# Optimization experiments

Measured on AMD Instinct MI355X. Metric: run time of the kernel, lower is better.

Reference implementation:

```python
import jax, jax.numpy as jnp
import numpy as np

B, LQ, LK = 16, 1024, 2048
E, F, A = 512, 256, 512


def setup_inputs() -> dict:
    key = jax.random.key(0)
    ks = jax.random.split(key, 8)
    s_e = 1.0 / np.sqrt(E)
    s_f = 1.0 / np.sqrt(F)
    s_a = 1.0 / np.sqrt(A)
    return {
        "lstm_embeddings": jax.random.normal(ks[0], (B, LQ, E), jnp.float32),
        "optical_flow_features": jax.random.normal(ks[1], (B, LK, F), jnp.float32),
        "Wq": jax.random.normal(ks[2], (E, A), jnp.float32) * s_e,
        "bq": jnp.zeros((A,), jnp.float32),
        "Wk": jax.random.normal(ks[3], (F, A), jnp.float32) * s_f,
        "bk": jnp.zeros((A,), jnp.float32),
        "Wv": jax.random.normal(ks[4], (F, A), jnp.float32) * s_f,
        "bv": jnp.zeros((A,), jnp.float32),
        "Wo": jax.random.normal(ks[5], (A, E), jnp.float32) * s_a,
        "bo": jnp.zeros((E,), jnp.float32),
    }


def reference(lstm_embeddings, optical_flow_features, Wq, bq, Wk, bk, Wv, bv, Wo, bo):
    # Linear projections (x @ W + b), matching nn.Linear with W stored as [in, out]
    q = lstm_embeddings @ Wq + bq            # [B, LQ, A]
    k = optical_flow_features @ Wk + bk      # [B, LK, A]
    v = optical_flow_features @ Wv + bv      # [B, LK, A]
    # NOTE: original module does NOT scale scores by 1/sqrt(A) — stay faithful.
    scores = jnp.einsum("bqa,bka->bqk", q, k)      # [B, LQ, LK]
    weights = jax.nn.softmax(scores, axis=-1)
    context = jnp.einsum("bqk,bka->bqa", weights, v)  # [B, LQ, A]
    return context @ Wo + bo                          # [B, LQ, E]
```

## Files before the change

kernel.cpp:

```cpp
#include <hip/hip_runtime.h>


#define DEV static __device__ __forceinline__

typedef __attribute__((ext_vector_type(8))) short s8v;
typedef __attribute__((ext_vector_type(8))) _Float16 h8v;
typedef __attribute__((ext_vector_type(4))) _Float16 h4v;
typedef __attribute__((ext_vector_type(4))) float f4v;
typedef __attribute__((ext_vector_type(16))) float f16f;
typedef __attribute__((ext_vector_type(4))) float float4v;
typedef unsigned short u16;
typedef unsigned int u32;

constexpr int BB = 16;
constexpr int LQ = 1024;
constexpr int LK = 2048;
constexpr int E = 512;
constexpr int F = 256;

DEV u16 f2bf(float x) {
    u32 u = __builtin_bit_cast(u32, x);
    u += 0x7fff + ((u >> 16) & 1);
    return (u16)(u >> 16);
}
DEV float bf2f(u16 h) { return __builtin_bit_cast(float, (u32)h << 16); }

DEV f4v MF(s8v a, s8v b, f4v c) {
    return __builtin_amdgcn_mfma_f32_16x16x32_bf16(a, b, c, 0, 0, 0);
}
DEV f4v MF16(h8v a, h8v b, f4v c) {
    return __builtin_amdgcn_mfma_f32_16x16x32_f16(a, b, c, 0, 0, 0);
}
DEV f16f MF32(h8v a, h8v b, f16f c) {
    return __builtin_amdgcn_mfma_f32_32x32x16_f16(a, b, c, 0, 0, 0);
}

__global__ __launch_bounds__(256) void wgemm(
    const float* __restrict__ Wq, const float* __restrict__ bq,
    const float* __restrict__ Wk, const float* __restrict__ Wv,
    const float* __restrict__ bv, const float* __restrict__ Wo,
    const float* __restrict__ bo,
    u16* __restrict__ Mhb, u16* __restrict__ Ntb,
    float* __restrict__ wvec, float* __restrict__ cvec)
{
    const int bi = blockIdx.x;
    const int tid = threadIdx.x;
    if (bi >= 64) {
        if (bi == 64) {
            const float* r = Wk + (size_t)tid * 512;
            float s = 0.f;
#pragma unroll 4
            for (int a = 0; a < 512; a += 4) {
                float4v v = *(const float4v*)(r + a);
                float4v bb = *(const float4v*)(bq + a);
                s += v[0] * bb[0] + v[1] * bb[1] + v[2] * bb[2] + v[3] * bb[3];
            }
            wvec[tid] = s;
        } else {
            int e = (bi - 65) * 256 + tid;
            float s = bo[e];
#pragma unroll 4
            for (int a = 0; a < 512; ++a) s += bv[a] * Wo[(size_t)a * 512 + e];
            cvec[e] = s;
        }
        return;
    }
    const bool ntm = bi >= 32;
    const int bj = ntm ? bi - 32 : bi;
    const int m0 = ntm ? (bj >> 2) * 64 : (bj >> 3) * 64;
    const int n0 = ntm ? (bj & 3) * 64 : (bj & 7) * 64;
    const float* Ag = ntm ? Wo : Wk;
    const float* Bg = ntm ? Wv : Wq;

    __shared__ u16 Ash[64][40], Asl[64][40];
    __shared__ u16 Bsh[64][40], Bsl[64][40];

    const int w = tid >> 6, lane = tid & 63;
    const int g = lane >> 4, qn = lane & 15;
    const int wr = w & 1, wc = w >> 1;

    f4v acc[2][2];
#pragma unroll
    for (int i = 0; i < 2; ++i)
#pragma unroll
        for (int j = 0; j < 2; ++j) acc[i][j] = (f4v){0.f, 0.f, 0.f, 0.f};

    for (int k0 = 0; k0 < 512; k0 += 32) {
        __syncthreads();
        if (!ntm) {
            int r = tid & 63, c = (tid >> 6) * 8;
            const float* s = Ag + (size_t)(m0 + r) * 512 + k0 + c;
            float4v v0 = *(const float4v*)s, v1 = *(const float4v*)(s + 4);
            short hh[8], ll[8];
#pragma unroll
            for (int i = 0; i < 8; ++i) {
                float x = (i < 4) ? v0[i] : v1[i - 4];
                u16 h = f2bf(x);
                hh[i] = (short)h;
                ll[i] = (short)f2bf(x - bf2f(h));
            }
            *(s8v*)&Ash[r][c] = (s8v){hh[0],hh[1],hh[2],hh[3],hh[4],hh[5],hh[6],hh[7]};
            *(s8v*)&Asl[r][c] = (s8v){ll[0],ll[1],ll[2],ll[3],ll[4],ll[5],ll[6],ll[7]};
        } else {
            int k = tid >> 3, mc = (tid & 7) * 8;
            const float* s = Ag + (size_t)(k0 + k) * 512 + m0 + mc;
            float4v v0 = *(const float4v*)s, v1 = *(const float4v*)(s + 4);
#pragma unroll
            for (int i = 0; i < 8; ++i) {
                float x = (i < 4) ? v0[i] : v1[i - 4];
                u16 h = f2bf(x);
                Ash[mc + i][k] = h;
                Asl[mc + i][k] = f2bf(x - bf2f(h));
            }
        }
        {
            int r = tid & 63, c = (tid >> 6) * 8;
            const float* s = Bg + (size_t)(n0 + r) * 512 + k0 + c;
            float4v v0 = *(const float4v*)s, v1 = *(const float4v*)(s + 4);
            short hh[8], ll[8];
#pragma unroll
            for (int i = 0; i < 8; ++i) {
                float x = (i < 4) ? v0[i] : v1[i - 4];
                u16 h = f2bf(x);
                hh[i] = (short)h;
                ll[i] = (short)f2bf(x - bf2f(h));
            }
            *(s8v*)&Bsh[r][c] = (s8v){hh[0],hh[1],hh[2],hh[3],hh[4],hh[5],hh[6],hh[7]};
            *(s8v*)&Bsl[r][c] = (s8v){ll[0],ll[1],ll[2],ll[3],ll[4],ll[5],ll[6],ll[7]};
        }
        __syncthreads();

        s8v ah[2], al[2], bh[2], bl[2];
#pragma unroll
        for (int mt = 0; mt < 2; ++mt) {
            ah[mt] = *(const s8v*)&Ash[wr * 32 + mt * 16 + qn][g * 8];
            al[mt] = *(const s8v*)&Asl[wr * 32 + mt * 16 + qn][g * 8];
        }
#pragma unroll
        for (int nt = 0; nt < 2; ++nt) {
            bh[nt] = *(const s8v*)&Bsh[wc * 32 + nt * 16 + qn][g * 8];
            bl[nt] = *(const s8v*)&Bsl[wc * 32 + nt * 16 + qn][g * 8];
        }
#pragma unroll
        for (int mt = 0; mt < 2; ++mt)
#pragma unroll
            for (int nt = 0; nt < 2; ++nt) {
                acc[mt][nt] = MF(ah[mt], bh[nt], acc[mt][nt]);
                acc[mt][nt] = MF(ah[mt], bl[nt], acc[mt][nt]);
                acc[mt][nt] = MF(al[mt], bh[nt], acc[mt][nt]);
            }
    }

#pragma unroll
    for (int mt = 0; mt < 2; ++mt)
#pragma unroll
        for (int nt = 0; nt < 2; ++nt)
#pragma unroll
            for (int r = 0; r < 4; ++r) {
                int gm = m0 + wr * 32 + mt * 16 + 4 * g + r;
                int gn = n0 + wc * 32 + nt * 16 + qn;
                float v = acc[mt][nt][r];
                if (!ntm) {
                    size_t off = (size_t)((gn >> 5) * 16 + (gm >> 4)) * 512 +
                                 (gm & 15) * 8 + ((gn >> 3) & 3) * 128 + (gn & 7);
                    Mhb[off] = __builtin_bit_cast(u16, (_Float16)v);
                } else {
                    size_t off = (size_t)((gn >> 5) * 32 + (gm >> 4)) * 512 +
                                 (gm & 15) * 8 + ((gn >> 3) & 3) * 128 + (gn & 7);
                    Ntb[off] = __builtin_bit_cast(u16, (_Float16)v);
                }
            }
}

__global__ __launch_bounds__(256) void prep16s(
    const float* __restrict__ y, _Float16* __restrict__ yA,
    _Float16* __restrict__ yB)
{
    __shared__ float Y[32][260];
    const int tid = threadIdx.x;
    const int b = blockIdx.y, t = blockIdx.x;
    const float* src = y + ((size_t)b * LK + t * 32) * F;
#pragma unroll
    for (int i = 0; i < 8; ++i) {
        int base = i * 1024 + tid * 4;
        int k = base >> 8, f = base & 255;
        *(float4v*)&Y[k][f] = *(const float4v*)(src + base);
    }
    __syncthreads();
    size_t tb = (size_t)(b * 64 + t) * 8192;
#pragma unroll
    for (int i = 0; i < 4; ++i) {
        int c = i * 256 + tid;
        int k = c & 31, hi = (c >> 5) & 1, fs = c >> 6;
        int f0 = fs * 16 + hi * 8;
        float4v v0 = *(const float4v*)&Y[k][f0];
        float4v v1 = *(const float4v*)&Y[k][f0 + 4];
        h8v v;
#pragma unroll
        for (int j = 0; j < 4; ++j) { v[j] = (_Float16)v0[j]; v[4 + j] = (_Float16)v1[j]; }
        *(h8v*)(yA + tb + (size_t)c * 8) = v;
    }
#pragma unroll
    for (int i = 0; i < 4; ++i) {
        int c = i * 256 + tid;
        int fl = c & 31, hi = (c >> 5) & 1, frag = c >> 6;
        int ft = frag >> 1, ks = frag & 1;
        int f = ft * 32 + fl, k0 = ks * 16 + hi * 8;
        h8v v;
#pragma unroll
        for (int j = 0; j < 8; ++j) v[j] = (_Float16)Y[k0 + j][f];
        *(h8v*)(yB + tb + (size_t)c * 8) = v;
    }
}

__global__ __launch_bounds__(256) void qprime4(
    const float* __restrict__ x, const u16* __restrict__ Mhb,
    const float* __restrict__ wv, _Float16* __restrict__ q16)
{
    __shared__ _Float16 Xs[2][128][40];
    const int tid = threadIdx.x, w = tid >> 6, lane = tid & 63;
    const int g = lane >> 4, qn = lane & 15;
    const int m0 = blockIdx.x * 128;
    const int nh = blockIdx.y * 8;
    const int srow = tid >> 1, scol = (tid & 1) * 16;
    const _Float16* Mh = (const _Float16*)Mhb;

    f4v acc[2][8];
#pragma unroll
    for (int i = 0; i < 2; ++i)
#pragma unroll
        for (int j = 0; j < 8; ++j) acc[i][j] = (f4v){0.f, 0.f, 0.f, 0.f};

    float4v a0, a1, a2, a3;
    auto LDA = [&](int k0) {
        const float* s = x + (size_t)(m0 + srow) * 512 + k0 + scol;
        a0 = *(const float4v*)s;      a1 = *(const float4v*)(s + 4);
        a2 = *(const float4v*)(s + 8); a3 = *(const float4v*)(s + 12);
    };
    auto STA = [&](int buf) {
        h8v v0, v1;
#pragma unroll
        for (int j = 0; j < 4; ++j) {
            v0[j] = (_Float16)a0[j]; v0[4 + j] = (_Float16)a1[j];
            v1[j] = (_Float16)a2[j]; v1[4 + j] = (_Float16)a3[j];
        }
        *(h8v*)&Xs[buf][srow][scol] = v0;
        *(h8v*)&Xs[buf][srow][scol + 8] = v1;
    };

    LDA(0); STA(0); LDA(32);
    __syncthreads();

    for (int t = 0; t < 16; ++t) {
        const int cur = t & 1;
        h8v af[2];
#pragma unroll
        for (int mt = 0; mt < 2; ++mt)
            af[mt] = *(const h8v*)&Xs[cur][(w * 2 + mt) * 16 + qn][g * 8];
        const int fb = t * 16 + nh;
#pragma unroll
        for (int nt = 0; nt < 8; ++nt) {
            h8v bf = *(const h8v*)(Mh + (size_t)(fb + nt) * 512 + lane * 8);
            acc[0][nt] = MF16(af[0], bf, acc[0][nt]);
            acc[1][nt] = MF16(af[1], bf, acc[1][nt]);
        }
        if (t < 15) {
            STA(cur ^ 1);
            if (t < 14) LDA((t + 2) * 32);
            __syncthreads();
        }
    }

#pragma unroll
    for (int mt = 0; mt < 2; ++mt)
#pragma unroll
        for (int nt = 0; nt < 8; ++nt) {
            int col = (nh + nt) * 16 + qn;
            float wvc = wv[col];
#pragma unroll
            for (int r = 0; r < 4; ++r) {
                int row = m0 + w * 32 + mt * 16 + 4 * g + r;
                q16[(size_t)row * 256 + col] = (_Float16)(acc[mt][nt][r] + wvc);
            }
        }
}

__global__ __launch_bounds__(512) void flash3(
    const _Float16* __restrict__ q16, const _Float16* __restrict__ yA,
    const _Float16* __restrict__ yB, _Float16* __restrict__ part,
    float* __restrict__ ml)
{
    __shared__ _Float16 Asb[8192];
    __shared__ _Float16 Bsb[8192];
    __shared__ _Float16 Pls[8][1024];

    const int tid = threadIdx.x;
    const int w = tid >> 6, lane = tid & 63;
    const int q32 = lane & 31, hi = lane >> 5;

    int id = blockIdx.x;
    int xcd = id & 7, slot = id >> 3;
    int grp = xcd + 8 * (slot >> 2);
    int qb = slot & 3;
    int b = grp >> 2, z = grp & 3;
    const int qw = qb * 256 + w * 32;

    h8v qf[16];
    {
        const _Float16* qp = q16 + ((size_t)b * LQ + qw + q32) * 256 + hi * 8;
#pragma unroll
        for (int s = 0; s < 16; ++s) qf[s] = *(const h8v*)(qp + s * 16);
    }
    f16f ctx[8];
#pragma unroll
    for (int i = 0; i < 8; ++i) ctx[i] = (f16f){};
    float mrun = -3.0e38f, lrun = 0.f;

    const size_t tbe = (size_t)(b * 64 + z * 16) * 8192;
    h8v sA0, sA1, sB0, sB1;
    auto LD = [&](int t) {
        const h8v* pa = (const h8v*)(yA + tbe + (size_t)t * 8192);
        const h8v* pb = (const h8v*)(yB + tbe + (size_t)t * 8192);
        sA0 = pa[tid]; sA1 = pa[tid + 512];
        sB0 = pb[tid]; sB1 = pb[tid + 512];
    };
    auto ST = [&]() {
        ((h8v*)Asb)[tid] = sA0; ((h8v*)Asb)[tid + 512] = sA1;
        ((h8v*)Bsb)[tid] = sB0; ((h8v*)Bsb)[tid + 512] = sB1;
    };

    LD(0); ST(); LD(1);
    __syncthreads();

    for (int t = 0; t < 16; ++t) {
        f16f S = (f16f){};
#pragma unroll
        for (int fs = 0; fs < 16; ++fs) {
            h8v a = *(const h8v*)(Asb + fs * 512 + lane * 8);
            S = MF32(a, qf[fs], S);
        }
        float mt = S[0];
#pragma unroll
        for (int r = 1; r < 16; ++r) mt = fmaxf(mt, S[r]);
        mt = fmaxf(mt, __shfl_xor(mt, 32));
        if (!__all(mt <= mrun + 8.f)) {
            float mnew = fmaxf(mrun, mt);
            float alpha = __expf(mrun - mnew);
            lrun *= alpha;
#pragma unroll
            for (int r = 0; r < 16; ++r) {
                int qr = (r & 3) + 8 * (r >> 2) + 4 * hi;
                float ar = __shfl(alpha, qr);
#pragma unroll
                for (int ft = 0; ft < 8; ++ft) ctx[ft][r] *= ar;
            }
            mrun = mnew;
        }
        float p[16], ps = 0.f;
#pragma unroll
        for (int r = 0; r < 16; ++r) { p[r] = __expf(S[r] - mrun); ps += p[r]; }
        ps += __shfl_xor(ps, 32);
        lrun += ps;
        {
            _Float16* pw = &Pls[w][0];
#pragma unroll
            for (int r2 = 0; r2 < 4; ++r2) {
                h4v pk = (h4v){(_Float16)p[4 * r2], (_Float16)p[4 * r2 + 1],
                               (_Float16)p[4 * r2 + 2], (_Float16)p[4 * r2 + 3]};
                *(h4v*)(pw + (r2 >> 1) * 512 + (r2 & 1) * 256 + q32 * 8 + hi * 4) = pk;
            }
        }
#pragma unroll
        for (int ks = 0; ks < 2; ++ks) {
            h8v pa = *(const h8v*)(&Pls[w][ks * 512] + lane * 8);
#pragma unroll
            for (int ft = 0; ft < 8; ++ft) {
                h8v bf = *(const h8v*)(Bsb + (ft * 2 + ks) * 512 + lane * 8);
                ctx[ft] = MF32(pa, bf, ctx[ft]);
            }
        }
        __syncthreads();
        if (t < 15) {
            ST();
            if (t < 14) LD(t + 2);
            __syncthreads();
        }
    }

    float linv = 1.f / lrun;
    _Float16* pp = part + ((size_t)z * (BB * LQ) + (size_t)b * LQ + qw) * 256;
#pragma unroll
    for (int r = 0; r < 16; ++r) {
        int qr = (r & 3) + 8 * (r >> 2) + 4 * hi;
        float ir = __shfl(linv, qr);
#pragma unroll
        for (int ft = 0; ft < 8; ++ft)
            pp[(size_t)qr * 256 + ft * 32 + q32] = (_Float16)(ctx[ft][r] * ir);
    }
    if (hi == 0) {
        size_t mi = (size_t)z * (BB * LQ) + (size_t)b * LQ + qw + q32;
        ml[2 * mi + 0] = mrun;
        ml[2 * mi + 1] = lrun;
    }
}

__global__ __launch_bounds__(256) void gemm2c(
    const _Float16* __restrict__ part, const float* __restrict__ ml,
    const u16* __restrict__ Ntb, const float* __restrict__ cvec,
    float* __restrict__ out)
{
    __shared__ _Float16 Asb[64][40];
    __shared__ float scl[64][4];
    const int tid = threadIdx.x;
    const int w = tid >> 6, lane = tid & 63;
    const int g = lane >> 4, qn = lane & 15;
    const int wr = w >> 1, wc = w & 1;
    const int m0 = blockIdx.x * 64, e0 = blockIdx.y * 256;
    constexpr size_t PL = (size_t)BB * LQ * F;
    constexpr size_t PR = (size_t)BB * LQ;

    if (tid < 64) {
        size_t i = m0 + tid;
        float m0v = ml[2 * i], l0v = ml[2 * i + 1];
        float m1v = ml[2 * (PR + i)], l1v = ml[2 * (PR + i) + 1];
        float m2v = ml[2 * (2 * PR + i)], l2v = ml[2 * (2 * PR + i) + 1];
        float m3v = ml[2 * (3 * PR + i)], l3v = ml[2 * (3 * PR + i) + 1];
        float M = fmaxf(fmaxf(m0v, m1v), fmaxf(m2v, m3v));
        float e0v = __expf(m0v - M), e1v = __expf(m1v - M);
        float e2v = __expf(m2v - M), e3v = __expf(m3v - M);
        float inv = 1.f / (l0v * e0v + l1v * e1v + l2v * e2v + l3v * e3v);
        scl[tid][0] = l0v * e0v * inv;
        scl[tid][1] = l1v * e1v * inv;
        scl[tid][2] = l2v * e2v * inv;
        scl[tid][3] = l3v * e3v * inv;
    }

    f4v acc[2][8];
#pragma unroll
    for (int i = 0; i < 2; ++i)
#pragma unroll
        for (int j = 0; j < 8; ++j) acc[i][j] = (f4v){0.f, 0.f, 0.f, 0.f};

    for (int k0 = 0; k0 < F; k0 += 32) {
        __syncthreads();
        {
            int r = tid & 63, c = (tid >> 6) * 8;
            size_t base = (size_t)(m0 + r) * F + k0 + c;
            h8v p0 = *(const h8v*)(part + base);
            h8v p1 = *(const h8v*)(part + PL + base);
            h8v p2 = *(const h8v*)(part + 2 * PL + base);
            h8v p3 = *(const h8v*)(part + 3 * PL + base);
            float s0 = scl[r][0], s1 = scl[r][1], s2 = scl[r][2], s3 = scl[r][3];
#pragma unroll
            for (int i = 0; i < 8; ++i) {
                float v = (float)p0[i] * s0 + (float)p1[i] * s1 +
                          (float)p2[i] * s2 + (float)p3[i] * s3;
                Asb[r][c + i] = (_Float16)v;
            }
        }
        __syncthreads();

        h8v ah[2], bh[8];
#pragma unroll
        for (int mt = 0; mt < 2; ++mt)
            ah[mt] = *(const h8v*)&Asb[wr * 32 + mt * 16 + qn][g * 8];
        int eb = (e0 + wc * 128) >> 4;
#pragma unroll
        for (int nt = 0; nt < 8; ++nt)
            bh[nt] = *(const h8v*)((const _Float16*)Ntb +
                     (size_t)((k0 >> 5) * 32 + eb + nt) * 512 + lane * 8);
#pragma unroll
        for (int mt = 0; mt < 2; ++mt)
#pragma unroll
            for (int nt = 0; nt < 8; ++nt)
                acc[mt][nt] = MF16(ah[mt], bh[nt], acc[mt][nt]);
    }

#pragma unroll
    for (int mt = 0; mt < 2; ++mt)
#pragma unroll
        for (int nt = 0; nt < 8; ++nt)
#pragma unroll
            for (int r = 0; r < 4; ++r) {
                int gm = m0 + wr * 32 + mt * 16 + 4 * g + r;
                int gn = e0 + wc * 128 + nt * 16 + qn;
                out[(size_t)gm * E + gn] = acc[mt][nt][r] + cvec[gn];
            }
}

extern "C" void kernel_launch(void* const* d_in, const int* in_sizes, int n_in,
                              void* d_out, int out_size, void* d_ws, size_t ws_size,
                              hipStream_t stream)
{
    const float* x  = (const float*)d_in[0];
    const float* y  = (const float*)d_in[1];
    const float* Wq = (const float*)d_in[2];
    const float* bq = (const float*)d_in[3];
    const float* Wk = (const float*)d_in[4];
    const float* Wv = (const float*)d_in[6];
    const float* bv = (const float*)d_in[7];
    const float* Wo = (const float*)d_in[8];
    const float* bo = (const float*)d_in[9];
    float* out = (float*)d_out;

    char* ws = (char*)d_ws;
    size_t off = 0;
    auto alloc = [&](size_t bytes) -> char* {
        char* p = ws + off;
        off = (off + bytes + 255) & ~(size_t)255;
        return p;
    };
    u16* Mhb  = (u16*)alloc(sizeof(u16) * F * E);
    float* wvec = (float*)alloc(sizeof(float) * F);
    float* cvec = (float*)alloc(sizeof(float) * E);
    u16* Ntb  = (u16*)alloc(sizeof(u16) * E * F);
    _Float16* q16 = (_Float16*)alloc(sizeof(u16) * (size_t)BB * LQ * F);
    _Float16* yA  = (_Float16*)alloc(sizeof(u16) * (size_t)BB * LK * F);
    _Float16* yB  = (_Float16*)alloc(sizeof(u16) * (size_t)BB * LK * F);
    _Float16* part = (_Float16*)alloc(sizeof(u16) * 4 * (size_t)BB * LQ * F);
    float* ml = (float*)alloc(sizeof(float) * 2 * 4 * (size_t)BB * LQ);
    (void)ws_size; (void)in_sizes; (void)n_in; (void)out_size;

    wgemm<<<dim3(67), dim3(256), 0, stream>>>(
        Wq, bq, Wk, Wv, bv, Wo, bo, Mhb, Ntb, wvec, cvec);
    prep16s<<<dim3(LK / 32, BB), dim3(256), 0, stream>>>(y, yA, yB);
    qprime4<<<dim3(BB * LQ / 128, 2), dim3(256), 0, stream>>>(x, Mhb, wvec, q16);
    flash3<<<dim3(256), dim3(512), 0, stream>>>(q16, yA, yB, part, ml);
    gemm2c<<<dim3(BB * LQ / 64, E / 256), dim3(256), 0, stream>>>(
        part, ml, Ntb, cvec, out);
}
```

Before: 138.7 us.

## Merge weight and y-prep kernels; double-buffer flash tiles via global_load_lds

The weight GEMM kernel and the y fp16 conversion kernel are fused into one launch, so a kernel boundary and the small serial weight work are removed. The flash attention kernel now stages two key tiles per step into double-buffered LDS using direct global-to-LDS loads, issued one stage ahead. This replaces the register-staged load/store with one barrier per pair of tiles, aiming to overlap memory with MFMA work. In exchange LDS use grows to about 144KB, which may limit occupancy, and the code relies on the async loads finishing before the single barrier.

```diff
diff --git a/kernel.cpp b/kernel.cpp
--- a/kernel.cpp
+++ b/kernel.cpp
@@ -35,7 +35,15 @@
     return __builtin_amdgcn_mfma_f32_32x32x16_f16(a, b, c, 0, 0, 0);
 }
 
-__global__ __launch_bounds__(256) void wgemm(
+DEV void gll16(const _Float16* g, _Float16* l) {
+    __builtin_amdgcn_global_load_lds(
+        (const __attribute__((address_space(1))) u32*)g,
+        (__attribute__((address_space(3))) u32*)l, 16, 0, 0);
+}
+
+__global__ __launch_bounds__(256) void prew(
+    const float* __restrict__ y, _Float16* __restrict__ yA,
+    _Float16* __restrict__ yB,
     const float* __restrict__ Wq, const float* __restrict__ bq,
     const float* __restrict__ Wk, const float* __restrict__ Wv,
     const float* __restrict__ bv, const float* __restrict__ Wo,
@@ -43,10 +51,51 @@
     u16* __restrict__ Mhb, u16* __restrict__ Ntb,
     float* __restrict__ wvec, float* __restrict__ cvec)
 {
+    __shared__ __align__(16) char smem[33536];
+    const int tid = threadIdx.x;
     const int bi = blockIdx.x;
-    const int tid = threadIdx.x;
-    if (bi >= 64) {
-        if (bi == 64) {
+
+    if (bi < 1024) {
+        float (*Y)[260] = (float(*)[260])smem;
+        const int b = bi >> 6, t = bi & 63;
+        const float* src = y + ((size_t)b * LK + t * 32) * F;
+#pragma unroll
+        for (int i = 0; i < 8; ++i) {
+            int base = i * 1024 + tid * 4;
+            int k = base >> 8, f = base & 255;
+            *(float4v*)&Y[k][f] = *(const float4v*)(src + base);
+        }
+        __syncthreads();
+        size_t tb = (size_t)(b * 64 + t) * 8192;
+#pragma unroll
+        for (int i = 0; i < 4; ++i) {
+            int c = i * 256 + tid;
+            int k = c & 31, hi = (c >> 5) & 1, fs = c >> 6;
+            int f0 = fs * 16 + hi * 8;
+            float4v v0 = *(const float4v*)&Y[k][f0];
+            float4v v1 = *(const float4v*)&Y[k][f0 + 4];
+            h8v v;
+#pragma unroll
+            for (int j = 0; j < 4; ++j) { v[j] = (_Float16)v0[j]; v[4 + j] = (_Float16)v1[j]; }
+            *(h8v*)(yA + tb + (size_t)c * 8) = v;
+        }
+#pragma unroll
+        for (int i = 0; i < 4; ++i) {
+            int c = i * 256 + tid;
+            int fl = c & 31, hi = (c >> 5) & 1, frag = c >> 6;
+            int ft = frag >> 1, ks = frag & 1;
+            int f = ft * 32 + fl, k0 = ks * 16 + hi * 8;
+            h8v v;
+#pragma unroll
+            for (int j = 0; j < 8; ++j) v[j] = (_Float16)Y[k0 + j][f];
+            *(h8v*)(yB + tb + (size_t)c * 8) = v;
+        }
+        return;
+    }
+
+    const int wb = bi - 1024;
+    if (wb >= 64) {
+        if (wb == 64) {
             const float* r = Wk + (size_t)tid * 512;
             float s = 0.f;
 #pragma unroll 4
@@ -57,7 +106,7 @@
             }
             wvec[tid] = s;
         } else {
-            int e = (bi - 65) * 256 + tid;
+            int e = (wb - 65) * 256 + tid;
             float s = bo[e];
 #pragma unroll 4
             for (int a = 0; a < 512; ++a) s += bv[a] * Wo[(size_t)a * 512 + e];
@@ -65,15 +114,18 @@
         }
         return;
     }
-    const bool ntm = bi >= 32;
-    const int bj = ntm ? bi - 32 : bi;
+
+    const bool ntm = wb >= 32;
+    const int bj = ntm ? wb - 32 : wb;
     const int m0 = ntm ? (bj >> 2) * 64 : (bj >> 3) * 64;
     const int n0 = ntm ? (bj & 3) * 64 : (bj & 7) * 64;
     const float* Ag = ntm ? Wo : Wk;
     const float* Bg = ntm ? Wv : Wq;
 
-    __shared__ u16 Ash[64][40], Asl[64][40];
-    __shared__ u16 Bsh[64][40], Bsl[64][40];
+    u16 (*Ash)[40] = (u16(*)[40])(smem);
+    u16 (*Asl)[40] = (u16(*)[40])(smem + 5120);
+    u16 (*Bsh)[40] = (u16(*)[40])(smem + 10240);
+    u16 (*Bsl)[40] = (u16(*)[40])(smem + 15360);
 
     const int w = tid >> 6, lane = tid & 63;
     const int g = lane >> 4, qn = lane & 15;
@@ -172,47 +224,6 @@
             }
 }
 
-__global__ __launch_bounds__(256) void prep16s(
-    const float* __restrict__ y, _Float16* __restrict__ yA,
-    _Float16* __restrict__ yB)
-{
-    __shared__ float Y[32][260];
-    const int tid = threadIdx.x;
-    const int b = blockIdx.y, t = blockIdx.x;
-    const float* src = y + ((size_t)b * LK + t * 32) * F;
-#pragma unroll
-    for (int i = 0; i < 8; ++i) {
-        int base = i * 1024 + tid * 4;
-        int k = base >> 8, f = base & 255;
-        *(float4v*)&Y[k][f] = *(const float4v*)(src + base);
-    }
-    __syncthreads();
-    size_t tb = (size_t)(b * 64 + t) * 8192;
-#pragma unroll
-    for (int i = 0; i < 4; ++i) {
-        int c = i * 256 + tid;
-        int k = c & 31, hi = (c >> 5) & 1, fs = c >> 6;
-        int f0 = fs * 16 + hi * 8;
-        float4v v0 = *(const float4v*)&Y[k][f0];
-        float4v v1 = *(const float4v*)&Y[k][f0 + 4];
-        h8v v;
-#pragma unroll
-        for (int j = 0; j < 4; ++j) { v[j] = (_Float16)v0[j]; v[4 + j] = (_Float16)v1[j]; }
-        *(h8v*)(yA + tb + (size_t)c * 8) = v;
-    }
-#pragma unroll
-    for (int i = 0; i < 4; ++i) {
-        int c = i * 256 + tid;
-        int fl = c & 31, hi = (c >> 5) & 1, frag = c >> 6;
-        int ft = frag >> 1, ks = frag & 1;
-        int f = ft * 32 + fl, k0 = ks * 16 + hi * 8;
-        h8v v;
-#pragma unroll
-        for (int j = 0; j < 8; ++j) v[j] = (_Float16)Y[k0 + j][f];
-        *(h8v*)(yB + tb + (size_t)c * 8) = v;
-    }
-}
-
 __global__ __launch_bounds__(256) void qprime4(
     const float* __restrict__ x, const u16* __restrict__ Mhb,
     const float* __restrict__ wv, _Float16* __restrict__ q16)
@@ -285,13 +296,13 @@
         }
 }
 
-__global__ __launch_bounds__(512) void flash3(
+__global__ __launch_bounds__(512) void flash5(
     const _Float16* __restrict__ q16, const _Float16* __restrict__ yA,
     const _Float16* __restrict__ yB, _Float16* __restrict__ part,
     float* __restrict__ ml)
 {
-    __shared__ _Float16 Asb[8192];
-    __shared__ _Float16 Bsb[8192];
+    __shared__ _Float16 Asb[2][2][8192];
+    __shared__ _Float16 Bsb[2][2][8192];
     __shared__ _Float16 Pls[8][1024];
 
     const int tid = threadIdx.x;
@@ -317,74 +328,78 @@
     float mrun = -3.0e38f, lrun = 0.f;
 
     const size_t tbe = (size_t)(b * 64 + z * 16) * 8192;
-    h8v sA0, sA1, sB0, sB1;
-    auto LD = [&](int t) {
-        const h8v* pa = (const h8v*)(yA + tbe + (size_t)t * 8192);
-        const h8v* pb = (const h8v*)(yB + tbe + (size_t)t * 8192);
-        sA0 = pa[tid]; sA1 = pa[tid + 512];
-        sB0 = pb[tid]; sB1 = pb[tid + 512];
+
+    auto STAGE = [&](int sup, int buf) {
+#pragma unroll
+        for (int j = 0; j < 2; ++j) {
+            const _Float16* ga = yA + tbe + (size_t)(sup * 2 + j) * 8192 + tid * 8;
+            const _Float16* gb = yB + tbe + (size_t)(sup * 2 + j) * 8192 + tid * 8;
+            gll16(ga,        &Asb[buf][j][tid * 8]);
+            gll16(ga + 4096, &Asb[buf][j][tid * 8 + 4096]);
+            gll16(gb,        &Bsb[buf][j][tid * 8]);
+            gll16(gb + 4096, &Bsb[buf][j][tid * 8 + 4096]);
+        }
     };
-    auto ST = [&]() {
-        ((h8v*)Asb)[tid] = sA0; ((h8v*)Asb)[tid + 512] = sA1;
-        ((h8v*)Bsb)[tid] = sB0; ((h8v*)Bsb)[tid + 512] = sB1;
-    };
-
-    LD(0); ST(); LD(1);
+
+    STAGE(0, 0);
     __syncthreads();
 
-    for (int t = 0; t < 16; ++t) {
-        f16f S = (f16f){};
-#pragma unroll
-        for (int fs = 0; fs < 16; ++fs) {
-            h8v a = *(const h8v*)(Asb + fs * 512 + lane * 8);
-            S = MF32(a, qf[fs], S);
-        }
-        float mt = S[0];
-#pragma unroll
-        for (int r = 1; r < 16; ++r) mt = fmaxf(mt, S[r]);
-        mt = fmaxf(mt, __shfl_xor(mt, 32));
-        if (!__all(mt <= mrun + 8.f)) {
-            float mnew = fmaxf(mrun, mt);
-            float alpha = __expf(mrun - mnew);
-            lrun *= alpha;
-#pragma unroll
-            for (int r = 0; r < 16; ++r) {
-                int qr = (r & 3) + 8 * (r >> 2) + 4 * hi;
-                float ar = __shfl(alpha, qr);
-#pragma unroll
-                for (int ft = 0; ft < 8; ++ft) ctx[ft][r] *= ar;
-            }
-            mrun = mnew;
-        }
-        float p[16], ps = 0.f;
-#pragma unroll
-        for (int r = 0; r < 16; ++r) { p[r] = __expf(S[r] - mrun); ps += p[r]; }
-        ps += __shfl_xor(ps, 32);
-        lrun += ps;
-        {
-            _Float16* pw = &Pls[w][0];
-#pragma unroll
-            for (int r2 = 0; r2 < 4; ++r2) {
-                h4v pk = (h4v){(_Float16)p[4 * r2], (_Float16)p[4 * r2 + 1],
-                               (_Float16)p[4 * r2 + 2], (_Float16)p[4 * r2 + 3]};
-                *(h4v*)(pw + (r2 >> 1) * 512 + (r2 & 1) * 256 + q32 * 8 + hi * 4) = pk;
-            }
-        }
-#pragma unroll
-        for (int ks = 0; ks < 2; ++ks) {
-            h8v pa = *(const h8v*)(&Pls[w][ks * 512] + lane * 8);
-#pragma unroll
-            for (int ft = 0; ft < 8; ++ft) {
-                h8v bf = *(const h8v*)(Bsb + (ft * 2 + ks) * 512 + lane * 8);
-                ctx[ft] = MF32(pa, bf, ctx[ft]);
+    int buf = 0;
+    for (int s = 0; s < 8; ++s) {
+        if (s < 7) STAGE(s + 1, buf ^ 1);
+#pragma unroll
+        for (int j = 0; j < 2; ++j) {
+            const _Float16* Ap = &Asb[buf][j][0];
+            const _Float16* Bp = &Bsb[buf][j][0];
+            f16f S = (f16f){};
+#pragma unroll
+            for (int fs = 0; fs < 16; ++fs) {
+                h8v a = *(const h8v*)(Ap + fs * 512 + lane * 8);
+                S = MF32(a, qf[fs], S);
+            }
+            float mt = S[0];
+#pragma unroll
+            for (int r = 1; r < 16; ++r) mt = fmaxf(mt, S[r]);
+            mt = fmaxf(mt, __shfl_xor(mt, 32));
+            if (!__all(mt <= mrun + 8.f)) {
+                float mnew = fmaxf(mrun, mt);
+                float alpha = __expf(mrun - mnew);
+                lrun *= alpha;
+#pragma unroll
+                for (int r = 0; r < 16; ++r) {
+                    int qr = (r & 3) + 8 * (r >> 2) + 4 * hi;
+                    float ar = __shfl(alpha, qr);
+#pragma unroll
+                    for (int ft = 0; ft < 8; ++ft) ctx[ft][r] *= ar;
+                }
+                mrun = mnew;
+            }
+            float p[16], ps = 0.f;
+#pragma unroll
+            for (int r = 0; r < 16; ++r) { p[r] = __expf(S[r] - mrun); ps += p[r]; }
+            ps += __shfl_xor(ps, 32);
+            lrun += ps;
+            {
+                _Float16* pw = &Pls[w][0];
+#pragma unroll
+                for (int r2 = 0; r2 < 4; ++r2) {
+                    h4v pk = (h4v){(_Float16)p[4 * r2], (_Float16)p[4 * r2 + 1],
+                                   (_Float16)p[4 * r2 + 2], (_Float16)p[4 * r2 + 3]};
+                    *(h4v*)(pw + (r2 >> 1) * 512 + (r2 & 1) * 256 + q32 * 8 + hi * 4) = pk;
+                }
+            }
+#pragma unroll
+            for (int ks = 0; ks < 2; ++ks) {
+                h8v pa = *(const h8v*)(&Pls[w][ks * 512] + lane * 8);
+#pragma unroll
+                for (int ft = 0; ft < 8; ++ft) {
+                    h8v bf = *(const h8v*)(Bp + (ft * 2 + ks) * 512 + lane * 8);
+                    ctx[ft] = MF32(pa, bf, ctx[ft]);
+                }
             }
         }
         __syncthreads();
-        if (t < 15) {
-            ST();
-            if (t < 14) LD(t + 2);
-            __syncthreads();
-        }
+        buf ^= 1;
     }
 
     float linv = 1.f / lrun;
@@ -521,11 +536,10 @@
     float* ml = (float*)alloc(sizeof(float) * 2 * 4 * (size_t)BB * LQ);
     (void)ws_size; (void)in_sizes; (void)n_in; (void)out_size;
 
-    wgemm<<<dim3(67), dim3(256), 0, stream>>>(
-        Wq, bq, Wk, Wv, bv, Wo, bo, Mhb, Ntb, wvec, cvec);
-    prep16s<<<dim3(LK / 32, BB), dim3(256), 0, stream>>>(y, yA, yB);
+    prew<<<dim3(1091), dim3(256), 0, stream>>>(
+        y, yA, yB, Wq, bq, Wk, Wv, bv, Wo, bo, Mhb, Ntb, wvec, cvec);
     qprime4<<<dim3(BB * LQ / 128, 2), dim3(256), 0, stream>>>(x, Mhb, wvec, q16);
-    flash3<<<dim3(256), dim3(512), 0, stream>>>(q16, yA, yB, part, ml);
+    flash5<<<dim3(256), dim3(512), 0, stream>>>(q16, yA, yB, part, ml);
     gemm2c<<<dim3(BB * LQ / 64, E / 256), dim3(256), 0, stream>>>(
         part, ml, Ntb, cvec, out);
 }
```

Measured after the change: 137.3 us. No clear change (-1.0%).
